# Kernel tuning notes

Hardware: AMD Instinct MI355X
Metric: run time of the kernel (lower is better)

The kernel has to match this reference:

```python
import jax, jax.numpy as jnp
import numpy as np

B, C_IN, N_PTS = 16, 4, 4096
N_P, DIM = 32, 256
EPS = 1e-5


def conv1d(x, w, b):
    # 1x1 Conv1d: x (B,C,N), w (O,C), b (O)
    return jnp.einsum('bcn,oc->bon', x, w) + b[None, :, None]


def bn(x, g, be):
    # BatchNorm1d in training mode: batch statistics over (B, N)
    m = jnp.mean(x, axis=(0, 2), keepdims=True)
    v = jnp.var(x, axis=(0, 2), keepdims=True)
    return g[None, :, None] * (x - m) * jax.lax.rsqrt(v + EPS) + be[None, :, None]


def softpool(x, n_p=N_P):
    # x: (B, C, N). For each sorting channel c, take indices of its top n_p
    # points and gather ALL C feature channels at those points.
    _, idx = jax.lax.top_k(x, n_p)            # (B, C_sort, n_p) indices into N
    g = jax.vmap(lambda xb, ib: xb[:, ib])(x, idx)  # (B, C_feat, C_sort, n_p)
    return jnp.transpose(g, (0, 1, 3, 2))     # (B, C_feat, n_p, C_sort)


def _forward(x, w1, b1, g1, be1, w2, b2, g2, be2, w3, b3, g3, be3,
             w8, b8, w9, b9, w4, b4, g4, be4, w5, b5, g5, be5,
             w6, b6, g6, be6, w7, b7):
    h = jax.nn.relu(bn(conv1d(x, w1, b1), g1, be1))      # (B,64,N)
    pointfeat = h
    h = jax.nn.relu(bn(conv1d(h, w2, b2), g2, be2))      # (B,128,N)
    h = bn(conv1d(h, w3, b3), g3, be3)                   # (B,256,N)
    sp = softpool(h)                                     # (B,256,32,256)
    # conv8: Conv2d(256,256,(1,256)) -> (B,256,32)
    y = jnp.einsum('bchw,ocw->boh', sp, w8) + b8[None, :, None]
    # conv9: Conv2d(256,256,(32,1)) -> (B,256)
    y = jnp.einsum('bch,och->bo', y, w9) + b9[None, :]
    glob = jnp.broadcast_to(y[:, :, None], (x.shape[0], DIM, x.shape[2]))
    h = jnp.concatenate([glob, pointfeat], axis=1)       # (B,320,N)
    h = jax.nn.relu(bn(conv1d(h, w4, b4), g4, be4))      # (B,512,N)
    h = jax.nn.relu(bn(conv1d(h, w5, b5), g5, be5))      # (B,256,N)
    h = jax.nn.relu(bn(conv1d(h, w6, b6), g6, be6))      # (B,128,N)
    return jnp.tanh(conv1d(h, w7, b7))                   # (B,3,N)


def setup_inputs() -> dict:
    key = jax.random.key(0)
    ks = iter(jax.random.split(key, 64))
    def p(shape, scale=0.05):
        return (jax.random.normal(next(ks), shape, jnp.float32) * scale)
    inp = {}
    inp['x'] = jax.random.normal(next(ks), (B, C_IN, N_PTS), jnp.float32)
    for name, o, i in [('1', 64, 4), ('2', 128, 64), ('3', 256, 128),
                       ('4', 512, 320), ('5', 256, 512), ('6', 128, 256)]:
        inp['w' + name] = p((o, i))
        inp['b' + name] = p((o,))
        inp['g' + name] = jnp.ones((o,), jnp.float32)
        inp['be' + name] = jnp.zeros((o,), jnp.float32)
    inp['w7'] = p((3, 128)); inp['b7'] = p((3,))
    inp['w8'] = p((DIM, DIM, DIM)); inp['b8'] = p((DIM,))
    inp['w9'] = p((DIM, DIM, N_P)); inp['b9'] = p((DIM,))
    return inp


def reference(x, w1, b1, g1, be1, w2, b2, g2, be2, w3, b3, g3, be3,
              w4, b4, g4, be4, w5, b5, g5, be5, w6, b6, g6, be6,
              w7, b7, w8, b8, w9, b9):
    return _forward(x, w1, b1, g1, be1, w2, b2, g2, be2, w3, b3, g3, be3,
                    w8, b8, w9, b9, w4, b4, g4, be4, w5, b5, g5, be5,
                    w6, b6, g6, be6, w7, b7)
```

## Files before the change

### kernel.cpp

```cpp
#include <hip/hip_runtime.h>
#include <cstdint>
#include <cstddef>

#define NPTS 4096
#define BATCH 16

typedef unsigned int uint32;
typedef unsigned long long u64;
typedef unsigned short u16;

typedef __attribute__((ext_vector_type(8))) short short8;
typedef __attribute__((ext_vector_type(16))) float float16;

__device__ __forceinline__ u16 f2bf(float f) {
  uint32 u = __float_as_uint(f);
  u = (u + 0x7fffu + ((u >> 16) & 1u)) >> 16;
  return (u16)u;
}
__device__ __forceinline__ float bf2f(u16 h) {
  return __uint_as_float(((uint32)h) << 16);
}

__global__ __launch_bounds__(256) void conv_gemm(
    const float* __restrict__ act, const float* __restrict__ wt,
    const float* __restrict__ rowbias, const float* __restrict__ obias,
    const float* __restrict__ inScale, const float* __restrict__ inShift,
    float* __restrict__ out, float* __restrict__ partials, int C, int O)
{
  __shared__ float As[16][68];
  __shared__ float Ws[16][68];
  __shared__ float redS[64][17];
  __shared__ float redQ[64][17];
  const int b  = blockIdx.z;
  const int o0 = blockIdx.y * 64;
  const int n0 = blockIdx.x * 64;
  const int t  = threadIdx.x;
  const int tx = t & 15, ty = t >> 4;
  float acc[4][4] = {};
  const float* actb = act + ((size_t)b * C) * NPTS;

  for (int k0 = 0; k0 < C; k0 += 16) {
    const int r  = ty;
    const int cs = tx * 4;
    const int k  = k0 + r;
    float4 av = make_float4(0.f, 0.f, 0.f, 0.f);
    if (k < C) {
      av = *(const float4*)(actb + (size_t)k * NPTS + n0 + cs);
      if (inScale) {
        const float scv = inScale[k], shv = inShift[k];
        av.x = fmaxf(fmaf(av.x, scv, shv), 0.f);
        av.y = fmaxf(fmaf(av.y, scv, shv), 0.f);
        av.z = fmaxf(fmaf(av.z, scv, shv), 0.f);
        av.w = fmaxf(fmaf(av.w, scv, shv), 0.f);
      }
    }
    *(float4*)&As[r][cs] = av;

    float4 wv = make_float4(0.f, 0.f, 0.f, 0.f);
    if (k < C) {
      const float* wp = wt + (size_t)k * O;
      const int o = o0 + cs;
      if (o + 3 < O) {
        wv = *(const float4*)&wp[o];
      } else {
        float tmp[4] = {0.f, 0.f, 0.f, 0.f};
        for (int j = 0; j < 4; ++j) if (o + j < O) tmp[j] = wp[o + j];
        wv = make_float4(tmp[0], tmp[1], tmp[2], tmp[3]);
      }
    }
    *(float4*)&Ws[r][cs] = wv;
    __syncthreads();

    const int kmax = (C - k0 < 16) ? (C - k0) : 16;
    for (int kk = 0; kk < kmax; ++kk) {
      float4 a = *(float4*)&As[kk][tx * 4];
      float4 w = *(float4*)&Ws[kk][ty * 4];
      acc[0][0] += w.x * a.x; acc[0][1] += w.x * a.y; acc[0][2] += w.x * a.z; acc[0][3] += w.x * a.w;
      acc[1][0] += w.y * a.x; acc[1][1] += w.y * a.y; acc[1][2] += w.y * a.z; acc[1][3] += w.y * a.w;
      acc[2][0] += w.z * a.x; acc[2][1] += w.z * a.y; acc[2][2] += w.z * a.z; acc[2][3] += w.z * a.w;
      acc[3][0] += w.w * a.x; acc[3][1] += w.w * a.y; acc[3][2] += w.w * a.z; acc[3][3] += w.w * a.w;
    }
    __syncthreads();
  }

  float s[4], q[4];
  for (int i = 0; i < 4; ++i) {
    const int o = o0 + ty * 4 + i;
    s[i] = 0.f; q[i] = 0.f;
    if (o >= O) continue;
    float base = 0.f;
    if (rowbias) base  = rowbias[(size_t)b * O + o];
    if (obias)   base += obias[o];
    float4 v = make_float4(acc[i][0] + base, acc[i][1] + base, acc[i][2] + base, acc[i][3] + base);
    *(float4*)&out[((size_t)b * O + o) * NPTS + n0 + tx * 4] = v;
    s[i] = v.x + v.y + v.z + v.w;
    q[i] = v.x * v.x + v.y * v.y + v.z * v.z + v.w * v.w;
  }

  if (partials) {
    for (int i = 0; i < 4; ++i) { redS[ty * 4 + i][tx] = s[i]; redQ[ty * 4 + i][tx] = q[i]; }
    __syncthreads();
    if (t < 64) {
      float a = 0.f;
      for (int j = 0; j < 16; ++j) a += redS[t][j];
      partials[((size_t)b * O + o0 + t) * 64 + blockIdx.x] = a;
    } else if (t < 128) {
      float a = 0.f;
      for (int j = 0; j < 16; ++j) a += redQ[t - 64][j];
      partials[(size_t)BATCH * O * 64 + ((size_t)b * O + o0 + t - 64) * 64 + blockIdx.x] = a;
    }
  }
}


__global__ __launch_bounds__(256) void conv1_f64(const float* __restrict__ x,
                                                 const float* __restrict__ w1,
                                                 float* __restrict__ h1f,
                                                 double* __restrict__ psd) {
  const int c = blockIdx.x, b = blockIdx.y;
  const double wa = (double)w1[c * 4 + 0], wb = (double)w1[c * 4 + 1];
  const double wc = (double)w1[c * 4 + 2], wd = (double)w1[c * 4 + 3];
  const float* xb = x + (size_t)b * 4 * NPTS;
  float* dst = h1f + ((size_t)b * 64 + c) * NPTS;
  double s = 0.0, q = 0.0;
  for (int n = threadIdx.x; n < NPTS; n += 256) {
    double v = wa * (double)xb[n] + wb * (double)xb[NPTS + n]
             + wc * (double)xb[2 * NPTS + n] + wd * (double)xb[3 * NPTS + n];
    dst[n] = (float)v;
    s += v; q += v * v;
  }
  __shared__ double ls[4], lq[4];
  for (int off = 32; off; off >>= 1) { s += __shfl_down(s, off, 64); q += __shfl_down(q, off, 64); }
  const int wid = threadIdx.x >> 6;
  if ((threadIdx.x & 63) == 0) { ls[wid] = s; lq[wid] = q; }
  __syncthreads();
  if (threadIdx.x == 0) {
    s = ls[0] + ls[1] + ls[2] + ls[3];
    q = lq[0] + lq[1] + lq[2] + lq[3];
    psd[(size_t)c * 16 + b] = s;
    psd[(size_t)64 * 16 + (size_t)c * 16 + b] = q;
  }
}

__global__ __launch_bounds__(256) void bn_finalize_f64(const double* __restrict__ psd,
                                                       const float* __restrict__ g,
                                                       const float* __restrict__ be,
                                                       double* __restrict__ scd, double* __restrict__ shd,
                                                       float* __restrict__ scf, float* __restrict__ shf,
                                                       int NT) {
  const int c = blockIdx.x;
  const int t = threadIdx.x;
  const double* p2 = psd + (size_t)gridDim.x * NT;
  const int k = (NT + 255) / 256;
  double s = 0.0, q = 0.0;
  for (int i = t * k; i < (t + 1) * k && i < NT; ++i) {
    s += psd[(size_t)c * NT + i];
    q += p2[(size_t)c * NT + i];
  }
  __shared__ double ss[256], qq[256];
  ss[t] = s; qq[t] = q;
  __syncthreads();
  if (t == 0) {
    double S = 0.0, Q = 0.0;
    for (int i = 0; i < 256; ++i) { S += ss[i]; Q += qq[i]; }
    const double m   = S * (1.0 / 65536.0);
    const double var = Q * (1.0 / 65536.0) - m * m;
    const double sc  = (double)g[c] / sqrt(var + 1e-5);
    const double sh  = (double)be[c] - m * sc;
    if (scd) { scd[c] = sc; shd[c] = sh; }
    scf[c] = (float)sc;
    shf[c] = (float)sh;
  }
}

__global__ __launch_bounds__(256) void pack_wtf64(const float* __restrict__ src,
                                                  double* __restrict__ dst,
                                                  int O, int C) {
  int i = blockIdx.x * 256 + threadIdx.x;
  if (i >= O * C) return;
  int c = i / O, o = i - c * O;
  dst[(size_t)c * O + o] = (double)src[(size_t)o * C + c];
}

__global__ __launch_bounds__(256) void conv2_f64v(
    const float* __restrict__ x, const float* __restrict__ w1,
    const double* __restrict__ w2t,
    const double* __restrict__ scd1, const double* __restrict__ shd1,
    double* __restrict__ h2d, double* __restrict__ psd)
{
  __shared__ double Bs[64][65];
  __shared__ double Ws[16][132];
  const int nb = blockIdx.x, b = blockIdx.y;
  const int n0 = nb * 64;
  const int t = threadIdx.x;
  const float* xb = x + (size_t)b * 4 * NPTS + n0;
  for (int i = t; i < 64 * 64; i += 256) {
    const int c1 = i >> 6, n = i & 63;
    double v = (double)w1[c1 * 4 + 0] * (double)xb[n]
             + (double)w1[c1 * 4 + 1] * (double)xb[NPTS + n]
             + (double)w1[c1 * 4 + 2] * (double)xb[2 * NPTS + n]
             + (double)w1[c1 * 4 + 3] * (double)xb[3 * NPTS + n];
    v = v * scd1[c1] + shd1[c1];
    Bs[c1][n] = v > 0.0 ? v : 0.0;
  }
  const int tx = t & 15, ty = t >> 4;
  double acc[8][4] = {};
  for (int ch = 0; ch < 4; ++ch) {
    __syncthreads();
    {
      const int r = t >> 4, oo = (t & 15) * 8;
      const double* srcw = w2t + (size_t)(ch * 16 + r) * 128 + oo;
#pragma unroll
      for (int j = 0; j < 8; ++j) Ws[r][oo + j] = srcw[j];
    }
    __syncthreads();
#pragma unroll
    for (int kk = 0; kk < 16; ++kk) {
      double a[8], bv[4];
#pragma unroll
      for (int j = 0; j < 8; ++j) a[j] = Ws[kk][ty * 8 + j];
#pragma unroll
      for (int j = 0; j < 4; ++j) bv[j] = Bs[ch * 16 + kk][tx + 16 * j];
#pragma unroll
      for (int i = 0; i < 8; ++i)
#pragma unroll
        for (int j = 0; j < 4; ++j) acc[i][j] = fma(a[i], bv[j], acc[i][j]);
    }
  }
  const size_t hb = (size_t)b * 128 * NPTS;
#pragma unroll
  for (int i = 0; i < 8; ++i) {
    const int o = ty * 8 + i;
    double s = 0.0, q = 0.0;
#pragma unroll
    for (int j = 0; j < 4; ++j) {
      const double v = acc[i][j];
      h2d[hb + (size_t)o * NPTS + n0 + tx + 16 * j] = v;
      s += v; q += v * v;
    }
#pragma unroll
    for (int m = 1; m < 16; m <<= 1) { s += __shfl_xor(s, m, 64); q += __shfl_xor(q, m, 64); }
    if (tx == 0) {
      psd[(size_t)o * 1024 + b * 64 + nb] = s;
      psd[(size_t)128 * 1024 + (size_t)o * 1024 + b * 64 + nb] = q;
    }
  }
}

__global__ __launch_bounds__(256) void conv3_f64v(
    const double* __restrict__ h2d, const double* __restrict__ w3t,
    const double* __restrict__ scd2, const double* __restrict__ shd2,
    double* __restrict__ h3d, double* __restrict__ psd)
{
  __shared__ double Bs[16][132];
  __shared__ double Ws[16][68];
  const int nb = blockIdx.x, og = blockIdx.y, b = blockIdx.z;
  const int n0 = nb * 128, o0 = og * 64;
  const int t = threadIdx.x;
  const int tx = t & 31, ty = t >> 5;
  const double* h2b = h2d + (size_t)b * 128 * NPTS;
  double acc[8][4] = {};
  for (int ch = 0; ch < 8; ++ch) {
    __syncthreads();
    {
      const int r = t >> 4, nn = (t & 15) * 8;
      const int c2 = ch * 16 + r;
      const double sc = scd2[c2], sh = shd2[c2];
      const double* srcr = h2b + (size_t)c2 * NPTS + n0 + nn;
#pragma unroll
      for (int j = 0; j < 8; ++j) {
        double v = srcr[j] * sc + sh;
        Bs[r][nn + j] = v > 0.0 ? v : 0.0;
      }
    }
    {
      const int r = t >> 4, oo = (t & 15) * 4;
      const double* srcw = w3t + (size_t)(ch * 16 + r) * 256 + o0 + oo;
#pragma unroll
      for (int j = 0; j < 4; ++j) Ws[r][oo + j] = srcw[j];
    }
    __syncthreads();
#pragma unroll
    for (int kk = 0; kk < 16; ++kk) {
      double a[8], bv[4];
#pragma unroll
      for (int j = 0; j < 8; ++j) a[j] = Ws[kk][ty * 8 + j];
#pragma unroll
      for (int j = 0; j < 4; ++j) bv[j] = Bs[kk][tx + 32 * j];
#pragma unroll
      for (int i = 0; i < 8; ++i)
#pragma unroll
        for (int j = 0; j < 4; ++j) acc[i][j] = fma(a[i], bv[j], acc[i][j]);
    }
  }
#pragma unroll
  for (int i = 0; i < 8; ++i) {
    const int o = o0 + ty * 8 + i;
    double s = 0.0, q = 0.0;
#pragma unroll
    for (int j = 0; j < 4; ++j) {
      const double v = acc[i][j];
      h3d[((size_t)b * 256 + o) * NPTS + n0 + tx + 32 * j] = v;
      s += v; q += v * v;
    }
#pragma unroll
    for (int m = 1; m < 32; m <<= 1) { s += __shfl_xor(s, m, 64); q += __shfl_xor(q, m, 64); }
    if (tx == 0) {
      psd[(size_t)o * 512 + b * 32 + nb] = s;
      psd[(size_t)256 * 512 + (size_t)o * 512 + b * 32 + nb] = q;
    }
  }
}

__global__ __launch_bounds__(256) void pack_wmfma(const float* __restrict__ src,
                                                  u16* __restrict__ ph, u16* __restrict__ pl,
                                                  int O, int Ctot, int cOff, int Csub) {
  int i = blockIdx.x * 256 + threadIdx.x;
  if (i >= O * Csub) return;
  const int KS = Csub >> 4;
  int j    = i & 7;
  int lj   = (i >> 3) & 63;
  int mtks = i >> 9;
  int ks   = mtks % KS;
  int mt   = mtks / KS;
  int o = mt * 32 + (lj & 31);
  int c = ks * 16 + (lj >> 5) * 8 + j;
  float v = src[(size_t)o * Ctot + cOff + c];
  u16 h = f2bf(v);
  ph[i] = h;
  pl[i] = f2bf(v - bf2f(h));
}

__global__ __launch_bounds__(256) void conv_mfma(
    const float* __restrict__ act, const u16* __restrict__ wh, const u16* __restrict__ wl,
    const float* __restrict__ rowbias,
    const float* __restrict__ inScale, const float* __restrict__ inShift,
    float* __restrict__ out, float* __restrict__ ps, int C, int O)
{
  __shared__ u16 Bh[2][4096];
  __shared__ u16 Bl[2][4096];
  const int b  = blockIdx.z;
  const int o0 = blockIdx.y * 128;
  const int n0 = blockIdx.x * 128;
  const int t  = threadIdx.x;
  const int l  = t & 63, wva = t >> 6;
  const int mt = blockIdx.y * 4 + wva;
  const int KS = C >> 4;
  const int NCH = C >> 5;
  const float* actb = act + ((size_t)b * C) * NPTS;

  float16 acc[4];
#pragma unroll
  for (int ns = 0; ns < 4; ++ns)
#pragma unroll
    for (int r = 0; r < 16; ++r) acc[ns][r] = 0.f;

  const int cq = t >> 5;
  const int nq = t & 31;
  const int nn = n0 + nq * 4;
  const int ksl = cq >> 2, oct = (cq >> 1) & 1, j0 = (cq & 1) * 4;

  float va[4][4];
  float4 scv = make_float4(1.f,1.f,1.f,1.f), shv = make_float4(0.f,0.f,0.f,0.f);

  auto loadChunk = [&](int ch) {
    const int cb = ch * 32 + cq * 4;
#pragma unroll
    for (int i2 = 0; i2 < 4; ++i2) {
      float4 v4 = *(const float4*)(actb + (size_t)(cb + i2) * NPTS + nn);
      va[i2][0] = v4.x; va[i2][1] = v4.y; va[i2][2] = v4.z; va[i2][3] = v4.w;
    }
    if (inScale) {
      scv = *(const float4*)&inScale[cb];
      shv = *(const float4*)&inShift[cb];
    }
  };
  auto applyBN = [&]() {
    if (!inScale) return;
#pragma unroll
    for (int d = 0; d < 4; ++d) {
      va[0][d] = fmaxf(fmaf(va[0][d], scv.x, shv.x), 0.f);
      va[1][d] = fmaxf(fmaf(va[1][d], scv.y, shv.y), 0.f);
      va[2][d] = fmaxf(fmaf(va[2][d], scv.z, shv.z), 0.f);
      va[3][d] = fmaxf(fmaf(va[3][d], scv.w, shv.w), 0.f);
    }
  };
  auto convWrite = [&](int buf) {
#pragma unroll
    for (int d = 0; d < 4; ++d) {
      const int nrel = nq * 4 + d;
      const int ns = nrel >> 5, li = nrel & 31;
      u16 h0 = f2bf(va[0][d]), h1 = f2bf(va[1][d]), h2 = f2bf(va[2][d]), h3 = f2bf(va[3][d]);
      u16 q0 = f2bf(va[0][d] - bf2f(h0));
      u16 q1 = f2bf(va[1][d] - bf2f(h1));
      u16 q2 = f2bf(va[2][d] - bf2f(h2));
      u16 q3 = f2bf(va[3][d] - bf2f(h3));
      const int idx = ((ksl * 4 + ns) * 64 + oct * 32 + li) * 8 + j0;
      *(ushort4*)&Bh[buf][idx] = make_ushort4(h0, h1, h2, h3);
      *(ushort4*)&Bl[buf][idx] = make_ushort4(q0, q1, q2, q3);
    }
  };

  loadChunk(0);
  applyBN();
  convWrite(0);
  __syncthreads();

  for (int ch = 0; ch < NCH; ++ch) {
    const size_t abase = (((size_t)mt * KS + ch * 2) * 64 + (size_t)l) * 8;
    short8 AH0 = *(const short8*)(wh + abase);
    short8 AH1 = *(const short8*)(wh + abase + 512);
    short8 AL0 = *(const short8*)(wl + abase);
    short8 AL1 = *(const short8*)(wl + abase + 512);
    const bool more = (ch + 1 < NCH);
    if (more) loadChunk(ch + 1);

    const u16* bh = Bh[ch & 1];
    const u16* bl = Bl[ch & 1];
#pragma unroll
    for (int ns = 0; ns < 4; ++ns) {
      short8 BH0 = *(const short8*)&bh[((0 * 4 + ns) * 64 + l) * 8];
      short8 BL0 = *(const short8*)&bl[((0 * 4 + ns) * 64 + l) * 8];
      acc[ns] = __builtin_amdgcn_mfma_f32_32x32x16_bf16(AL0, BH0, acc[ns], 0, 0, 0);
      acc[ns] = __builtin_amdgcn_mfma_f32_32x32x16_bf16(AH0, BL0, acc[ns], 0, 0, 0);
      acc[ns] = __builtin_amdgcn_mfma_f32_32x32x16_bf16(AH0, BH0, acc[ns], 0, 0, 0);
      short8 BH1 = *(const short8*)&bh[((4 + ns) * 64 + l) * 8];
      short8 BL1 = *(const short8*)&bl[((4 + ns) * 64 + l) * 8];
      acc[ns] = __builtin_amdgcn_mfma_f32_32x32x16_bf16(AL1, BH1, acc[ns], 0, 0, 0);
      acc[ns] = __builtin_amdgcn_mfma_f32_32x32x16_bf16(AH1, BL1, acc[ns], 0, 0, 0);
      acc[ns] = __builtin_amdgcn_mfma_f32_32x32x16_bf16(AH1, BH1, acc[ns], 0, 0, 0);
    }
    if (more) { applyBN(); convWrite((ch + 1) & 1); }
    __syncthreads();
  }

  const int col = l & 31, half = l >> 5;
  float sv[16], sq[16];
#pragma unroll
  for (int r = 0; r < 16; ++r) {
    const int o = o0 + wva * 32 + (r & 3) + 8 * (r >> 2) + 4 * half;
    const float base = rowbias ? rowbias[(size_t)b * O + o] : 0.f;
    float s = 0.f, q = 0.f;
#pragma unroll
    for (int ns = 0; ns < 4; ++ns) {
      float val = acc[ns][r] + base;
      out[((size_t)b * O + o) * NPTS + n0 + ns * 32 + col] = val;
      s += val; q += val * val;
    }
    sv[r] = s; sq[r] = q;
  }
  if (ps) {
#pragma unroll
    for (int r = 0; r < 16; ++r) {
#pragma unroll
      for (int m = 1; m < 32; m <<= 1) {
        sv[r] += __shfl_xor(sv[r], m, 64);
        sq[r] += __shfl_xor(sq[r], m, 64);
      }
    }
    if (col == 0) {
#pragma unroll
      for (int r = 0; r < 16; ++r) {
        const int o = o0 + wva * 32 + (r & 3) + 8 * (r >> 2) + 4 * half;
        ps[((size_t)b * O + o) * 32 + blockIdx.x] = sv[r];
        ps[(size_t)BATCH * O * 32 + ((size_t)b * O + o) * 32 + blockIdx.x] = sq[r];
      }
    }
  }
}

__global__ __launch_bounds__(256) void bn_finalize(const float* __restrict__ ps,
                                                   const float* __restrict__ g, const float* __restrict__ be,
                                                   float* __restrict__ scale, float* __restrict__ shift,
                                                   int O, int NT) {
  const int c = blockIdx.x;
  const int total = BATCH * NT;
  const float* p2 = ps + (size_t)BATCH * O * NT;
  const int t = threadIdx.x;
  float s = 0.f, q = 0.f;
  for (int e = t; e < total; e += 256) {
    const int b = e / NT, nt = e - b * NT;
    const size_t a = ((size_t)b * O + c) * NT + nt;
    s += ps[a];
    q += p2[a];
  }
#pragma unroll
  for (int m = 32; m; m >>= 1) {
    s += __shfl_down(s, m, 64);
    q += __shfl_down(q, m, 64);
  }
  __shared__ float lsS[4], lsQ[4];
  const int wid = t >> 6;
  if ((t & 63) == 0) { lsS[wid] = s; lsQ[wid] = q; }
  __syncthreads();
  if (t == 0) {
    s = lsS[0] + lsS[1] + lsS[2] + lsS[3];
    q = lsQ[0] + lsQ[1] + lsQ[2] + lsQ[3];
    const float inv = 1.f / 65536.f;
    float m   = s * inv;
    float var = q * inv - m * m;
    float sc  = g[c] * rsqrtf(var + 1e-5f);
    scale[c] = sc;
    shift[c] = be[c] - m * sc;
  }
}

__global__ __launch_bounds__(256) void topk_kernel(const double* __restrict__ h3,
                                                   int* __restrict__ idxp) {
  __shared__ u64 wl[4][32];
  const int c = blockIdx.x, b = blockIdx.y;
  const double* src = h3 + ((size_t)b * 256 + c) * NPTS;
  const int t = threadIdx.x;
  const int l = t & 63, w = t >> 6;
  const int base = w * 1024;

  u64 k[16];
  u64 bk = 0;
#pragma unroll
  for (int s = 0; s < 16; ++s) {
    const int ri = base + s * 64 + l;
    u64 u = (u64)__double_as_longlong(src[ri]);
    u64 m = ((long long)u < 0) ? ~u : (u | 0x8000000000000000ULL);
    m = (m & ~0xFFFULL) | (u64)(4095 - ri);
    k[s] = m;
    if (m > bk) bk = m;
  }

  for (int r = 0; r < 32; ++r) {
    u64 m = bk;
#pragma unroll
    for (int off = 1; off < 64; off <<= 1) {
      u64 o = __shfl_xor((unsigned long long)m, off, 64);
      if (o > m) m = o;
    }
    if (l == 0) wl[w][r] = m;
    const int ri = 4095 - (int)(m & 0xFFF);
    if ((ri & 63) == l) {
      const int slot = (ri >> 6) & 15;
#pragma unroll
      for (int s = 0; s < 16; ++s) if (s == slot) k[s] = 0;
      u64 m0 = k[0] > k[1] ? k[0] : k[1];
      u64 m1 = k[2] > k[3] ? k[2] : k[3];
      u64 m2 = k[4] > k[5] ? k[4] : k[5];
      u64 m3 = k[6] > k[7] ? k[6] : k[7];
      u64 m4 = k[8] > k[9] ? k[8] : k[9];
      u64 m5 = k[10] > k[11] ? k[10] : k[11];
      u64 m6 = k[12] > k[13] ? k[12] : k[13];
      u64 m7 = k[14] > k[15] ? k[14] : k[15];
      m0 = m0 > m1 ? m0 : m1;  m2 = m2 > m3 ? m2 : m3;
      m4 = m4 > m5 ? m4 : m5;  m6 = m6 > m7 ? m6 : m7;
      m0 = m0 > m2 ? m0 : m2;  m4 = m4 > m6 ? m4 : m6;
      bk = m0 > m4 ? m0 : m4;
    }
  }
  __syncthreads();

  if (t < 4) {
    int* dst = idxp + ((size_t)b * 256 + c) * 32;
    int cp = 0;
    u64 cv = wl[t][0];
    for (int r = 0; r < 32; ++r) {
      u64 mv = cv;
      u64 ov;
      ov = __shfl_xor((unsigned long long)mv, 1, 64); if (ov > mv) mv = ov;
      ov = __shfl_xor((unsigned long long)mv, 2, 64); if (ov > mv) mv = ov;
      if (t == 0) dst[r] = 4095 - (int)(mv & 0xFFF);
      if (mv == cv) {
        ++cp;
        cv = (cp < 32) ? wl[t][cp] : 0;
      }
    }
  }
}

__global__ __launch_bounds__(256) void transpose_h3(const double* __restrict__ h3,
                                                    float* __restrict__ h3T,
                                                    const float* __restrict__ sc,
                                                    const float* __restrict__ sh) {
  __shared__ double tile[32][33];
  const int b = blockIdx.z;
  const int n0 = blockIdx.x * 32, c0 = blockIdx.y * 32;
  const int tx = threadIdx.x & 31, ty = threadIdx.x >> 5;
  const double* src = h3 + (size_t)b * 256 * NPTS;
  for (int j = 0; j < 4; ++j)
    tile[ty + j * 8][tx] = src[(size_t)(c0 + ty + j * 8) * NPTS + n0 + tx];
  __syncthreads();
  float* dst = h3T + (size_t)b * NPTS * 256;
  const float scv = sc[c0 + tx], shv = sh[c0 + tx];
  for (int j = 0; j < 4; ++j)
    dst[(size_t)(n0 + ty + j * 8) * 256 + c0 + tx] = fmaf((float)tile[tx][ty + j * 8], scv, shv);
}

__global__ __launch_bounds__(256) void transpack_w8(const float* __restrict__ w8,
                                                    u16* __restrict__ w8h, u16* __restrict__ w8l) {
  __shared__ float tile[64][65];
  const int m0 = blockIdx.x * 64, w0 = blockIdx.y * 64;
  const int tx = threadIdx.x & 63, ty = threadIdx.x >> 6;
#pragma unroll
  for (int j = 0; j < 16; ++j)
    tile[ty + j * 4][tx] = w8[(size_t)(m0 + ty + j * 4) * 256 + w0 + tx];
  __syncthreads();
  const int m = m0 + tx;
  const int o = m >> 8, c = m & 255;
  const int mt = (o >> 5) & 7;
  const int lane = (o & 31) + ((c >> 3) & 1) * 32;
  const int ks = (c >> 4) & 15;
  const int jj = c & 7;
#pragma unroll
  for (int j = 0; j < 16; ++j) {
    const int w = w0 + ty + j * 4;
    float v = tile[tx][ty + j * 4];
    size_t f = ((((size_t)w * 8 + mt) * 16 + ks) * 64 + lane) * 8 + jj;
    u16 h = f2bf(v);
    w8h[f] = h;
    w8l[f] = f2bf(v - bf2f(h));
  }
}

#define Y8N (BATCH * 256 * 32)
__global__ __launch_bounds__(256, 1) void conv8_mfma(
    const float* __restrict__ h3T, const u16* __restrict__ w8h,
    const u16* __restrict__ w8l, const int* __restrict__ idxp,
    float* __restrict__ y8p)
{
  __shared__ u16 G[2][8192];
  const int wg = blockIdx.x;
  const int oq = blockIdx.y;
  const int bg = blockIdx.z;
  const int t  = threadIdx.x;
  const int l  = t & 63, wv = t >> 6;
  const int mt = oq * 4 + wv;

  float16 accH[4], accL[4];
  for (int i = 0; i < 4; ++i)
    for (int r = 0; r < 16; ++r) { accH[i][r] = 0.f; accL[i][r] = 0.f; }

  short8 ah[16], al[16];
  const int hrow  = t >> 3;
  const int cbase = (t & 7) * 32;
  float4 g4[8];

  auto issueG = [&](int step) {
    int wi = step >> 2, bi = step & 3;
    int w = wg * 8 + wi;
    int b = bg * 4 + bi;
    int n = idxp[((size_t)b * 256 + w) * 32 + hrow];
    const float* src = h3T + ((size_t)b * NPTS + n) * 256 + cbase;
#pragma unroll
    for (int j = 0; j < 8; ++j) g4[j] = *(const float4*)&src[j * 4];
  };
  auto writeG = [&](int buf) {
#pragma unroll
    for (int a = 0; a < 4; ++a) {
      int c8 = (cbase >> 3) + a;
      int ks = c8 >> 1;
      int lp = hrow + (c8 & 1) * 32;
      float4 v0 = g4[a * 2], v1 = g4[a * 2 + 1];
      uint32 u0 = (uint32)f2bf(v0.x) | ((uint32)f2bf(v0.y) << 16);
      uint32 u1 = (uint32)f2bf(v0.z) | ((uint32)f2bf(v0.w) << 16);
      uint32 u2 = (uint32)f2bf(v1.x) | ((uint32)f2bf(v1.y) << 16);
      uint32 u3 = (uint32)f2bf(v1.z) | ((uint32)f2bf(v1.w) << 16);
      *(uint4*)&G[buf][((size_t)ks * 64 + lp) * 8] = make_uint4(u0, u1, u2, u3);
    }
  };

  issueG(0); writeG(0);
  __syncthreads();

  for (int wi = 0; wi < 8; ++wi) {
    const int w = wg * 8 + wi;
    {
      const size_t base = (((size_t)w * 8 + mt) * 16) * 512 + (size_t)l * 8;
#pragma unroll
      for (int ks = 0; ks < 16; ++ks) {
        ah[ks] = *(const short8*)(w8h + base + ks * 512);
        al[ks] = *(const short8*)(w8l + base + ks * 512);
      }
    }
#pragma unroll
    for (int bi = 0; bi < 4; ++bi) {
      const int step = wi * 4 + bi;
      const int cur = bi & 1;
      if (step < 31) issueG(step + 1);
      const u16* Gc = G[cur];
#pragma unroll
      for (int ks = 0; ks < 16; ++ks) {
        short8 bf = *(const short8*)&Gc[((size_t)ks * 64 + l) * 8];
        accH[bi] = __builtin_amdgcn_mfma_f32_32x32x16_bf16(ah[ks], bf, accH[bi], 0, 0, 0);
        accL[bi] = __builtin_amdgcn_mfma_f32_32x32x16_bf16(al[ks], bf, accL[bi], 0, 0, 0);
      }
      if (step < 31) writeG(1 - cur);
      __syncthreads();
    }
  }

  const int h = l & 31;
  const int rbase = oq * 128 + wv * 32 + 4 * (l >> 5);
#pragma unroll
  for (int bi = 0; bi < 4; ++bi) {
    int b = bg * 4 + bi;
    float* dst = y8p + ((size_t)(wg * BATCH + b) * 256) * 32;
#pragma unroll
    for (int r = 0; r < 16; ++r) {
      int o = rbase + (r & 3) + 8 * (r >> 2);
      dst[(size_t)o * 32 + h] = accH[bi][r] + accL[bi][r];
    }
  }
}

__global__ __launch_bounds__(256) void y8_reduce(const float* __restrict__ y8p,
                                                 const float* __restrict__ b8,
                                                 float* __restrict__ y8) {
  int i = blockIdx.x * 256 + threadIdx.x;
  float s = b8[(i >> 5) & 255];
#pragma unroll
  for (int p = 0; p < 32; ++p) s += y8p[(size_t)p * Y8N + i];
  y8[i] = s;
}

__global__ __launch_bounds__(256) void conv9_kernel(const float* __restrict__ y8,
                                                    const float* __restrict__ w9,
                                                    const float* __restrict__ b9,
                                                    float* __restrict__ y9) {
  const int o = blockIdx.x, b = blockIdx.y;
  const float* yb = y8 + (size_t)b * 8192;
  const float* wo = w9 + (size_t)o * 8192;
  float s = 0.f;
  for (int i = threadIdx.x * 4; i < 8192; i += 1024) {
    float4 v = *(const float4*)&yb[i];
    float4 u = *(const float4*)&wo[i];
    s += v.x * u.x + v.y * u.y + v.z * u.z + v.w * u.w;
  }
  for (int off = 32; off; off >>= 1) s += __shfl_down(s, off, 64);
  __shared__ float ls[4];
  const int wid = threadIdx.x >> 6;
  if ((threadIdx.x & 63) == 0) ls[wid] = s;
  __syncthreads();
  if (threadIdx.x == 0) y9[(size_t)b * 256 + o] = ls[0] + ls[1] + ls[2] + ls[3] + b9[o];
}

__global__ __launch_bounds__(256) void cvec_kernel(const float* __restrict__ y9,
                                                   const float* __restrict__ w4,
                                                   float* __restrict__ cvec) {
  int tid = blockIdx.x * 256 + threadIdx.x;
  if (tid >= BATCH * 512) return;
  const int b = tid >> 9, o = tid & 511;
  const float* row = w4 + (size_t)o * 320;
  const float* yb  = y9 + (size_t)b * 256;
  float s = 0.f;
  for (int c = 0; c < 256; c += 4) {
    float4 u = *(const float4*)&row[c];
    s += u.x * yb[c] + u.y * yb[c + 1] + u.z * yb[c + 2] + u.w * yb[c + 3];
  }
  cvec[(size_t)b * 512 + o] = s;
}

__global__ __launch_bounds__(256) void transpose_w(const float* __restrict__ src,
                                                   float* __restrict__ dst,
                                                   int O, int Ctot, int cOff, int Csub) {
  int i = blockIdx.x * 256 + threadIdx.x;
  if (i >= O * Csub) return;
  int c = i / O, o = i - c * O;
  dst[(size_t)c * O + o] = src[(size_t)o * Ctot + cOff + c];
}

__global__ __launch_bounds__(256) void tanh_out(const float* __restrict__ raw,
                                                float* __restrict__ out) {
  int i = blockIdx.x * 256 + threadIdx.x;
  if (i < BATCH * 3 * NPTS) out[i] = tanhf(raw[i]);
}

extern "C" void kernel_launch(void* const* d_in, const int* in_sizes, int n_in,
                              void* d_out, int out_size, void* d_ws, size_t ws_size,
                              hipStream_t stream) {
  (void)in_sizes; (void)n_in; (void)ws_size; (void)out_size;
  const float* x   = (const float*)d_in[0];
  const float* w1  = (const float*)d_in[1];
  const float* g1  = (const float*)d_in[3];
  const float* be1 = (const float*)d_in[4];
  const float* w2  = (const float*)d_in[5];
  const float* g2  = (const float*)d_in[7];
  const float* be2 = (const float*)d_in[8];
  const float* w3  = (const float*)d_in[9];
  const float* g3  = (const float*)d_in[11];
  const float* be3 = (const float*)d_in[12];
  const float* w4  = (const float*)d_in[13];
  const float* g4  = (const float*)d_in[15];
  const float* be4 = (const float*)d_in[16];
  const float* w5  = (const float*)d_in[17];
  const float* g5  = (const float*)d_in[19];
  const float* be5 = (const float*)d_in[20];
  const float* w6  = (const float*)d_in[21];
  const float* g6  = (const float*)d_in[23];
  const float* be6 = (const float*)d_in[24];
  const float* w7  = (const float*)d_in[25];
  const float* b7  = (const float*)d_in[26];
  const float* w8  = (const float*)d_in[27];
  const float* b8  = (const float*)d_in[28];
  const float* w9  = (const float*)d_in[29];
  const float* b9  = (const float*)d_in[30];

  char* ws = (char*)d_ws;
  size_t off = 0;
  auto alloc = [&](size_t bytes) -> void* {
    void* p = ws + off;
    off += (bytes + 255) & ~(size_t)255;
    return p;
  };
  float* Q1  = (float*)alloc((size_t)BATCH * 64  * NPTS * 4);
  float* Q2  = (float*)alloc((size_t)BATCH * 128 * NPTS * 4);
  float* Q3  = (float*)alloc((size_t)BATCH * 256 * NPTS * 4);
  float* Q4  = (float*)alloc((size_t)BATCH * 256 * NPTS * 4);
  float* Q5  = (float*)alloc((size_t)BATCH * 256 * NPTS * 4);
  int*   idx  = (int*)alloc((size_t)BATCH * 256 * 32 * 4);
  float* y8   = (float*)alloc((size_t)Y8N * 4);
  float* y9   = (float*)alloc((size_t)BATCH * 256 * 4);
  float* cvec = (float*)alloc((size_t)BATCH * 512 * 4);
  float* ps   = (float*)alloc((size_t)2 * BATCH * 512 * 32 * 4);
  double* psd = (double*)alloc((size_t)2 * 256 * 1024 * 8);
  float* scb  = (float*)alloc((size_t)6 * 1024 * 4);
  double* scdb = (double*)alloc((size_t)1024 * 8);
  float* w7t  = (float*)alloc(128 * 3 * 4);
  u16* ph4 = (u16*)alloc(512 * 64  * 2);  u16* pl4 = (u16*)alloc(512 * 64  * 2);
  u16* ph5 = (u16*)alloc(256 * 512 * 2);  u16* pl5 = (u16*)alloc(256 * 512 * 2);
  u16* ph6 = (u16*)alloc(128 * 256 * 2);  u16* pl6 = (u16*)alloc(128 * 256 * 2);
  double* w2t = (double*)alloc((size_t)64 * 128 * 8);
  double* w3t = (double*)alloc((size_t)128 * 256 * 8);

  double* h2d = (double*)Q3;
  double* h3d = (double*)Q4;
  u16*   w8h = (u16*)Q4;
  u16*   w8l = (u16*)Q4 + (size_t)16777216;
  float* y8p = Q2;
  float* h4  = Q2;
  float* h5  = Q5;
  float* h6  = Q2;

  float* sc[6]; float* sh[6];
  for (int i = 0; i < 6; ++i) { sc[i] = scb + i * 1024; sh[i] = scb + i * 1024 + 512; }
  double* scd1 = scdb;        double* shd1 = scdb + 64;
  double* scd2 = scdb + 128;  double* shd2 = scdb + 256;

  transpose_w<<<(128 * 3 + 255) / 256, 256, 0, stream>>>(w7, w7t, 3, 128, 0, 128);
  pack_wmfma<<<(512 * 64  + 255) / 256, 256, 0, stream>>>(w4, ph4, pl4, 512, 320, 256, 64);
  pack_wmfma<<<(256 * 512 + 255) / 256, 256, 0, stream>>>(w5, ph5, pl5, 256, 512, 0,   512);
  pack_wmfma<<<(128 * 256 + 255) / 256, 256, 0, stream>>>(w6, ph6, pl6, 128, 256, 0,   256);
  pack_wtf64<<<(128 * 64 + 255) / 256,  256, 0, stream>>>(w2, w2t, 128, 64);
  pack_wtf64<<<(256 * 128 + 255) / 256, 256, 0, stream>>>(w3, w3t, 256, 128);

  conv1_f64<<<dim3(64, BATCH), 256, 0, stream>>>(x, w1, Q1, psd);
  bn_finalize_f64<<<64, 256, 0, stream>>>(psd, g1, be1, scd1, shd1, sc[0], sh[0], 16);
  conv2_f64v<<<dim3(64, BATCH), 256, 0, stream>>>(x, w1, w2t, scd1, shd1, h2d, psd);
  bn_finalize_f64<<<128, 256, 0, stream>>>(psd, g2, be2, scd2, shd2, sc[1], sh[1], 1024);
  conv3_f64v<<<dim3(32, 4, BATCH), 256, 0, stream>>>(h2d, w3t, scd2, shd2, h3d, psd);
  bn_finalize_f64<<<256, 256, 0, stream>>>(psd, g3, be3, nullptr, nullptr, sc[2], sh[2], 512);

  topk_kernel<<<dim3(256, BATCH), 256, 0, stream>>>(h3d, idx);
  transpose_h3<<<dim3(NPTS / 32, 8, BATCH), 256, 0, stream>>>(h3d, Q3, sc[2], sh[2]);

  transpack_w8<<<dim3(1024, 4), 256, 0, stream>>>(w8, w8h, w8l);

  conv8_mfma<<<dim3(32, 2, 4), 256, 0, stream>>>(Q3, w8h, w8l, idx, y8p);
  y8_reduce<<<Y8N / 256, 256, 0, stream>>>(y8p, b8, y8);
  conv9_kernel<<<dim3(256, BATCH), 256, 0, stream>>>(y8, w9, b9, y9);
  cvec_kernel<<<(BATCH * 512 + 255) / 256, 256, 0, stream>>>(y9, w4, cvec);

  conv_mfma<<<dim3(32, 4, BATCH), 256, 0, stream>>>(Q1, ph4, pl4, cvec, sc[0], sh[0], h4, ps, 64, 512);
  bn_finalize<<<512, 256, 0, stream>>>(ps, g4, be4, sc[3], sh[3], 512, 32);
  conv_mfma<<<dim3(32, 2, BATCH), 256, 0, stream>>>(h4, ph5, pl5, nullptr, sc[3], sh[3], h5, ps, 512, 256);
  bn_finalize<<<256, 256, 0, stream>>>(ps, g5, be5, sc[4], sh[4], 256, 32);
  conv_mfma<<<dim3(32, 1, BATCH), 256, 0, stream>>>(h5, ph6, pl6, nullptr, sc[4], sh[4], h6, ps, 256, 128);
  bn_finalize<<<128, 256, 0, stream>>>(ps, g6, be6, sc[5], sh[5], 128, 32);
  conv_gemm<<<dim3(64, 1, BATCH), 256, 0, stream>>>(h6, w7t, nullptr, b7, sc[5], sh[5], Q1, nullptr, 128, 3);
  tanh_out<<<(BATCH * 3 * NPTS) / 256, 256, 0, stream>>>(Q1, (float*)d_out);
}
```

Baseline: 862.6 us.

## Compute conv3 with split-bf16 MFMA and rerank fp32 top-k candidates in fp64

The fp64 SIMT conv3 GEMM is replaced by the existing split-bf16 MFMA conv kernel, which produces fp32 h3. Top-k now runs on the fp32 values to select 40 candidates per channel. Those candidates are then re-scored exactly in fp64 using a transposed h2 and the original w3, and the top 32 are picked from them. This trades a large fp64 GEMM for MFMA work plus a small rerank and extra transposes, and relies on 40 candidates being enough to recover the exact ordering.

```diff
diff --git a/kernel.cpp b/kernel.cpp
--- a/kernel.cpp
+++ b/kernel.cpp
@@ -186,7 +186,7 @@
     const float* __restrict__ x, const float* __restrict__ w1,
     const double* __restrict__ w2t,
     const double* __restrict__ scd1, const double* __restrict__ shd1,
-    double* __restrict__ h2d, double* __restrict__ psd)
+    double* __restrict__ h2d, float* __restrict__ h2f, double* __restrict__ psd)
 {
   __shared__ double Bs[64][65];
   __shared__ double Ws[16][132];
@@ -236,6 +236,7 @@
     for (int j = 0; j < 4; ++j) {
       const double v = acc[i][j];
       h2d[hb + (size_t)o * NPTS + n0 + tx + 16 * j] = v;
+      h2f[hb + (size_t)o * NPTS + n0 + tx + 16 * j] = (float)v;
       s += v; q += v * v;
     }
 #pragma unroll
@@ -243,71 +244,6 @@
     if (tx == 0) {
       psd[(size_t)o * 1024 + b * 64 + nb] = s;
       psd[(size_t)128 * 1024 + (size_t)o * 1024 + b * 64 + nb] = q;
-    }
-  }
-}
-
-__global__ __launch_bounds__(256) void conv3_f64v(
-    const double* __restrict__ h2d, const double* __restrict__ w3t,
-    const double* __restrict__ scd2, const double* __restrict__ shd2,
-    double* __restrict__ h3d, double* __restrict__ psd)
-{
-  __shared__ double Bs[16][132];
-  __shared__ double Ws[16][68];
-  const int nb = blockIdx.x, og = blockIdx.y, b = blockIdx.z;
-  const int n0 = nb * 128, o0 = og * 64;
-  const int t = threadIdx.x;
-  const int tx = t & 31, ty = t >> 5;
-  const double* h2b = h2d + (size_t)b * 128 * NPTS;
-  double acc[8][4] = {};
-  for (int ch = 0; ch < 8; ++ch) {
-    __syncthreads();
-    {
-      const int r = t >> 4, nn = (t & 15) * 8;
-      const int c2 = ch * 16 + r;
-      const double sc = scd2[c2], sh = shd2[c2];
-      const double* srcr = h2b + (size_t)c2 * NPTS + n0 + nn;
-#pragma unroll
-      for (int j = 0; j < 8; ++j) {
-        double v = srcr[j] * sc + sh;
-        Bs[r][nn + j] = v > 0.0 ? v : 0.0;
-      }
-    }
-    {
-      const int r = t >> 4, oo = (t & 15) * 4;
-      const double* srcw = w3t + (size_t)(ch * 16 + r) * 256 + o0 + oo;
-#pragma unroll
-      for (int j = 0; j < 4; ++j) Ws[r][oo + j] = srcw[j];
-    }
-    __syncthreads();
-#pragma unroll
-    for (int kk = 0; kk < 16; ++kk) {
-      double a[8], bv[4];
-#pragma unroll
-      for (int j = 0; j < 8; ++j) a[j] = Ws[kk][ty * 8 + j];
-#pragma unroll
-      for (int j = 0; j < 4; ++j) bv[j] = Bs[kk][tx + 32 * j];
-#pragma unroll
-      for (int i = 0; i < 8; ++i)
-#pragma unroll
-        for (int j = 0; j < 4; ++j) acc[i][j] = fma(a[i], bv[j], acc[i][j]);
-    }
-  }
-#pragma unroll
-  for (int i = 0; i < 8; ++i) {
-    const int o = o0 + ty * 8 + i;
-    double s = 0.0, q = 0.0;
-#pragma unroll
-    for (int j = 0; j < 4; ++j) {
-      const double v = acc[i][j];
-      h3d[((size_t)b * 256 + o) * NPTS + n0 + tx + 32 * j] = v;
-      s += v; q += v * v;
-    }
-#pragma unroll
-    for (int m = 1; m < 32; m <<= 1) { s += __shfl_xor(s, m, 64); q += __shfl_xor(q, m, 64); }
-    if (tx == 0) {
-      psd[(size_t)o * 512 + b * 32 + nb] = s;
-      psd[(size_t)256 * 512 + (size_t)o * 512 + b * 32 + nb] = q;
     }
   }
 }
@@ -505,11 +441,12 @@
   }
 }
 
-__global__ __launch_bounds__(256) void topk_kernel(const double* __restrict__ h3,
-                                                   int* __restrict__ idxp) {
-  __shared__ u64 wl[4][32];
+#define NCAND 40
+__global__ __launch_bounds__(256) void topk40_f32(const float* __restrict__ h3,
+                                                  int* __restrict__ cand) {
+  __shared__ u64 wl[4][NCAND];
   const int c = blockIdx.x, b = blockIdx.y;
-  const double* src = h3 + ((size_t)b * 256 + c) * NPTS;
+  const float* src = h3 + ((size_t)b * 256 + c) * NPTS;
   const int t = threadIdx.x;
   const int l = t & 63, w = t >> 6;
   const int base = w * 1024;
@@ -519,14 +456,14 @@
 #pragma unroll
   for (int s = 0; s < 16; ++s) {
     const int ri = base + s * 64 + l;
-    u64 u = (u64)__double_as_longlong(src[ri]);
-    u64 m = ((long long)u < 0) ? ~u : (u | 0x8000000000000000ULL);
-    m = (m & ~0xFFFULL) | (u64)(4095 - ri);
+    uint32 u = __float_as_uint(src[ri]);
+    uint32 m32 = ((int)u < 0) ? ~u : (u | 0x80000000u);
+    u64 m = ((u64)m32 << 32) | (u64)(4095 - ri);
     k[s] = m;
     if (m > bk) bk = m;
   }
 
-  for (int r = 0; r < 32; ++r) {
+  for (int r = 0; r < NCAND; ++r) {
     u64 m = bk;
 #pragma unroll
     for (int off = 1; off < 64; off <<= 1) {
@@ -534,7 +471,7 @@
       if (o > m) m = o;
     }
     if (l == 0) wl[w][r] = m;
-    const int ri = 4095 - (int)(m & 0xFFF);
+    const int ri = 4095 - (int)(m & 0xFFFu);
     if ((ri & 63) == l) {
       const int slot = (ri >> 6) & 15;
 #pragma unroll
@@ -556,39 +493,99 @@
   __syncthreads();
 
   if (t < 4) {
-    int* dst = idxp + ((size_t)b * 256 + c) * 32;
+    int* dst = cand + ((size_t)b * 256 + c) * NCAND;
     int cp = 0;
     u64 cv = wl[t][0];
-    for (int r = 0; r < 32; ++r) {
+    for (int r = 0; r < NCAND; ++r) {
       u64 mv = cv;
       u64 ov;
       ov = __shfl_xor((unsigned long long)mv, 1, 64); if (ov > mv) mv = ov;
       ov = __shfl_xor((unsigned long long)mv, 2, 64); if (ov > mv) mv = ov;
-      if (t == 0) dst[r] = 4095 - (int)(mv & 0xFFF);
+      if (t == 0) dst[r] = 4095 - (int)(mv & 0xFFFu);
       if (mv == cv) {
         ++cp;
-        cv = (cp < 32) ? wl[t][cp] : 0;
+        cv = (cp < NCAND) ? wl[t][cp] : 0;
       }
     }
   }
 }
 
-__global__ __launch_bounds__(256) void transpose_h3(const double* __restrict__ h3,
-                                                    float* __restrict__ h3T,
-                                                    const float* __restrict__ sc,
-                                                    const float* __restrict__ sh) {
+__global__ __launch_bounds__(256) void transpose_h2(const double* __restrict__ h2d,
+                                                    double* __restrict__ h2T) {
   __shared__ double tile[32][33];
   const int b = blockIdx.z;
   const int n0 = blockIdx.x * 32, c0 = blockIdx.y * 32;
   const int tx = threadIdx.x & 31, ty = threadIdx.x >> 5;
-  const double* src = h3 + (size_t)b * 256 * NPTS;
+  const double* src = h2d + (size_t)b * 128 * NPTS;
+  for (int j = 0; j < 4; ++j)
+    tile[ty + j * 8][tx] = src[(size_t)(c0 + ty + j * 8) * NPTS + n0 + tx];
+  __syncthreads();
+  double* dst = h2T + (size_t)b * NPTS * 128;
+  for (int j = 0; j < 4; ++j)
+    dst[(size_t)(n0 + ty + j * 8) * 128 + c0 + tx] = tile[tx][ty + j * 8];
+}
+
+__global__ __launch_bounds__(64) void rerank_f64(const double* __restrict__ h2T,
+                                                 const float* __restrict__ w3,
+                                                 const double* __restrict__ scd2,
+                                                 const double* __restrict__ shd2,
+                                                 const int* __restrict__ cand,
+                                                 int* __restrict__ idxp) {
+  __shared__ u64 keys[NCAND];
+  const int o = blockIdx.x, b = blockIdx.y;
+  const int l = threadIdx.x;
+  const double wA = (double)w3[(size_t)o * 128 + l];
+  const double wB = (double)w3[(size_t)o * 128 + l + 64];
+  const double sA = scd2[l],      hA = shd2[l];
+  const double sB = scd2[l + 64], hB = shd2[l + 64];
+  const int* cd = cand + ((size_t)b * 256 + o) * NCAND;
+  const double* hb = h2T + (size_t)b * NPTS * 128;
+  for (int kk = 0; kk < NCAND; ++kk) {
+    const int n = cd[kk];
+    const double* col = hb + (size_t)n * 128;
+    double va = col[l] * sA + hA;       va = va > 0.0 ? va : 0.0;
+    double vb = col[l + 64] * sB + hB;  vb = vb > 0.0 ? vb : 0.0;
+    double p = wA * va + wB * vb;
+#pragma unroll
+    for (int off = 32; off; off >>= 1) p += __shfl_down(p, off, 64);
+    if (l == 0) {
+      u64 u = (u64)__double_as_longlong(p);
+      u64 m = ((long long)u < 0) ? ~u : (u | 0x8000000000000000ULL);
+      m = (m & ~0xFFFULL) | (u64)(4095 - n);
+      keys[kk] = m;
+    }
+  }
+  __syncthreads();
+  u64 kv = (l < NCAND) ? keys[l] : 0;
+  int* dst = idxp + ((size_t)b * 256 + o) * 32;
+  for (int r = 0; r < 32; ++r) {
+    u64 m = kv;
+#pragma unroll
+    for (int off = 1; off < 64; off <<= 1) {
+      u64 o2 = __shfl_xor((unsigned long long)m, off, 64);
+      if (o2 > m) m = o2;
+    }
+    if (l == 0) dst[r] = 4095 - (int)(m & 0xFFFULL);
+    if (m == kv) kv = 0;
+  }
+}
+
+__global__ __launch_bounds__(256) void transpose_h3f(const float* __restrict__ h3,
+                                                     float* __restrict__ h3T,
+                                                     const float* __restrict__ sc,
+                                                     const float* __restrict__ sh) {
+  __shared__ float tile[32][33];
+  const int b = blockIdx.z;
+  const int n0 = blockIdx.x * 32, c0 = blockIdx.y * 32;
+  const int tx = threadIdx.x & 31, ty = threadIdx.x >> 5;
+  const float* src = h3 + (size_t)b * 256 * NPTS;
   for (int j = 0; j < 4; ++j)
     tile[ty + j * 8][tx] = src[(size_t)(c0 + ty + j * 8) * NPTS + n0 + tx];
   __syncthreads();
   float* dst = h3T + (size_t)b * NPTS * 256;
   const float scv = sc[c0 + tx], shv = sh[c0 + tx];
   for (int j = 0; j < 4; ++j)
-    dst[(size_t)(n0 + ty + j * 8) * 256 + c0 + tx] = fmaf((float)tile[tx][ty + j * 8], scv, shv);
+    dst[(size_t)(n0 + ty + j * 8) * 256 + c0 + tx] = fmaf(tile[tx][ty + j * 8], scv, shv);
 }
 
 __global__ __launch_bounds__(256) void transpack_w8(const float* __restrict__ w8,
@@ -813,6 +810,7 @@
   float* Q4  = (float*)alloc((size_t)BATCH * 256 * NPTS * 4);
   float* Q5  = (float*)alloc((size_t)BATCH * 256 * NPTS * 4);
   int*   idx  = (int*)alloc((size_t)BATCH * 256 * 32 * 4);
+  int*   cand = (int*)alloc((size_t)BATCH * 256 * NCAND * 4);
   float* y8   = (float*)alloc((size_t)Y8N * 4);
   float* y9   = (float*)alloc((size_t)BATCH * 256 * 4);
   float* cvec = (float*)alloc((size_t)BATCH * 512 * 4);
@@ -821,14 +819,16 @@
   float* scb  = (float*)alloc((size_t)6 * 1024 * 4);
   double* scdb = (double*)alloc((size_t)1024 * 8);
   float* w7t  = (float*)alloc(128 * 3 * 4);
+  u16* ph3 = (u16*)alloc(256 * 128 * 2);  u16* pl3 = (u16*)alloc(256 * 128 * 2);
   u16* ph4 = (u16*)alloc(512 * 64  * 2);  u16* pl4 = (u16*)alloc(512 * 64  * 2);
   u16* ph5 = (u16*)alloc(256 * 512 * 2);  u16* pl5 = (u16*)alloc(256 * 512 * 2);
   u16* ph6 = (u16*)alloc(128 * 256 * 2);  u16* pl6 = (u16*)alloc(128 * 256 * 2);
   double* w2t = (double*)alloc((size_t)64 * 128 * 8);
-  double* w3t = (double*)alloc((size_t)128 * 256 * 8);
 
   double* h2d = (double*)Q3;
-  double* h3d = (double*)Q4;
+  float*  h2f = (float*)Q5;
+  double* h2T = (double*)Q5;
+  float*  h3f = Q4;
   u16*   w8h = (u16*)Q4;
   u16*   w8l = (u16*)Q4 + (size_t)16777216;
   float* y8p = Q2;
@@ -842,21 +842,23 @@
   double* scd2 = scdb + 128;  double* shd2 = scdb + 256;
 
   transpose_w<<<(128 * 3 + 255) / 256, 256, 0, stream>>>(w7, w7t, 3, 128, 0, 128);
+  pack_wmfma<<<(256 * 128 + 255) / 256, 256, 0, stream>>>(w3, ph3, pl3, 256, 128, 0,   128);
   pack_wmfma<<<(512 * 64  + 255) / 256, 256, 0, stream>>>(w4, ph4, pl4, 512, 320, 256, 64);
   pack_wmfma<<<(256 * 512 + 255) / 256, 256, 0, stream>>>(w5, ph5, pl5, 256, 512, 0,   512);
   pack_wmfma<<<(128 * 256 + 255) / 256, 256, 0, stream>>>(w6, ph6, pl6, 128, 256, 0,   256);
   pack_wtf64<<<(128 * 64 + 255) / 256,  256, 0, stream>>>(w2, w2t, 128, 64);
-  pack_wtf64<<<(256 * 128 + 255) / 256, 256, 0, stream>>>(w3, w3t, 256, 128);
 
   conv1_f64<<<dim3(64, BATCH), 256, 0, stream>>>(x, w1, Q1, psd);
   bn_finalize_f64<<<64, 256, 0, stream>>>(psd, g1, be1, scd1, shd1, sc[0], sh[0], 16);
-  conv2_f64v<<<dim3(64, BATCH), 256, 0, stream>>>(x, w1, w2t, scd1, shd1, h2d, psd);
+  conv2_f64v<<<dim3(64, BATCH), 256, 0, stream>>>(x, w1, w2t, scd1, shd1, h2d, h2f, psd);
   bn_finalize_f64<<<128, 256, 0, stream>>>(psd, g2, be2, scd2, shd2, sc[1], sh[1], 1024);
-  conv3_f64v<<<dim3(32, 4, BATCH), 256, 0, stream>>>(h2d, w3t, scd2, shd2, h3d, psd);
-  bn_finalize_f64<<<256, 256, 0, stream>>>(psd, g3, be3, nullptr, nullptr, sc[2], sh[2], 512);
-
-  topk_kernel<<<dim3(256, BATCH), 256, 0, stream>>>(h3d, idx);
-  transpose_h3<<<dim3(NPTS / 32, 8, BATCH), 256, 0, stream>>>(h3d, Q3, sc[2], sh[2]);
+  conv_mfma<<<dim3(32, 2, BATCH), 256, 0, stream>>>(h2f, ph3, pl3, nullptr, sc[1], sh[1], h3f, ps, 128, 256);
+  bn_finalize<<<256, 256, 0, stream>>>(ps, g3, be3, sc[2], sh[2], 256, 32);
+
+  topk40_f32<<<dim3(256, BATCH), 256, 0, stream>>>(h3f, cand);
+  transpose_h2<<<dim3(NPTS / 32, 4, BATCH), 256, 0, stream>>>(h2d, h2T);
+  rerank_f64<<<dim3(256, BATCH), 64, 0, stream>>>(h2T, w3, scd2, shd2, cand, idx);
+  transpose_h3f<<<dim3(NPTS / 32, 8, BATCH), 256, 0, stream>>>(h3f, Q3, sc[2], sh[2]);
 
   transpack_w8<<<dim3(1024, 4), 256, 0, stream>>>(w8, w8h, w8l);
 
```

After: 856.7 us. Within noise of the previous version (-0.7%).
